# Performance work log

Hardware: AMD Instinct MI355X
Metric: run time of the kernel (lower is better)

## Reference

```python
import jax, jax.numpy as jnp
import numpy as np

B, D, H, O, E = 4096, 1024, 4096, 1024, 8
TOP_K = 2


def setup_inputs() -> dict:
    key = jax.random.key(0)
    ks = jax.random.split(key, 7)
    s = 0.02
    return {
        "expert_input": jax.random.normal(ks[0], (B, D), dtype=jnp.float32),
        "Wg": jax.random.normal(ks[1], (D, E), dtype=jnp.float32) * s,
        "bg": jnp.zeros((E,), dtype=jnp.float32),
        "W1": jax.random.normal(ks[2], (E, D, H), dtype=jnp.float32) * s,
        "b1": jnp.zeros((E, H), dtype=jnp.float32),
        "W2": jax.random.normal(ks[3], (E, H, O), dtype=jnp.float32) * s,
        "b2": jnp.zeros((E, O), dtype=jnp.float32),
    }


def reference(expert_input, Wg, bg, W1, b1, W2, b2):
    x = expert_input                                  # [B, D]
    gate_logits = x @ Wg + bg                         # [B, E]
    topk_logits, topk_idx = jax.lax.top_k(gate_logits, TOP_K)
    topk_w = jax.nn.softmax(topk_logits, axis=1)      # softmax over the k selected logits
    rows = jnp.arange(x.shape[0])[:, None]
    dense_w = jnp.zeros_like(gate_logits).at[rows, topk_idx].set(topk_w)  # [B, E]
    # Dense (all-experts) evaluation; zero gate weight == unrouted, so math
    # matches the masked per-expert loop in the torch module exactly.
    h = jax.nn.relu(jnp.einsum('bd,edh->ebh', x, W1) + b1[:, None, :])    # [E, B, H]
    expert_out = jnp.einsum('ebh,eho->ebo', h, W2) + b2[:, None, :]       # [E, B, O]
    routed = jnp.einsum('be,ebo->bo', dense_w, expert_out)                # [B, O]
    return routed
```

## Files before the change

kernel.cpp:

```cpp
#include <hip/hip_runtime.h>
#include <cstdint>

#define DEVI __device__ __forceinline__

typedef __bf16 bf16x8_t __attribute__((ext_vector_type(8)));
typedef float f32x4_t __attribute__((ext_vector_type(4)));

typedef const __attribute__((address_space(1))) unsigned int* gas_t;
typedef __attribute__((address_space(3))) unsigned int* las_t;

DEVI void glds16(const void* g, void* l) {
  __builtin_amdgcn_global_load_lds((gas_t)g, (las_t)l, 16, 0, 0);
}

DEVI uint16_t f2b(float f) {
  uint32_t u = __builtin_bit_cast(uint32_t, f);
  u += 0x7fffu + ((u >> 16) & 1u);
  return (uint16_t)(u >> 16);
}

DEVI f32x4_t ldsr(uint32_t addr) {
  f32x4_t r;
  asm volatile("ds_read_b128 %0, %1" : "=v"(r) : "v"(addr));
  return r;
}
DEVI f32x4_t ldsr_o(uint32_t addr, int imm) {
  f32x4_t r;
  switch (imm) {
    case 1024: asm volatile("ds_read_b128 %0, %1 offset:1024" : "=v"(r) : "v"(addr)); break;
    case 2048: asm volatile("ds_read_b128 %0, %1 offset:2048" : "=v"(r) : "v"(addr)); break;
    default:   asm volatile("ds_read_b128 %0, %1 offset:3072" : "=v"(r) : "v"(addr)); break;
  }
  return r;
}

static constexpr int MAXT = 72;

__global__ __launch_bounds__(256) void moe_gate(const float* __restrict__ x,
    const float* __restrict__ Wg, const float* __restrict__ bg,
    int* __restrict__ gidx, float* __restrict__ gw) {
  const int lane = threadIdx.x & 63;
  const int b = blockIdx.x * 4 + (threadIdx.x >> 6);
  float acc[8];
#pragma unroll
  for (int e = 0; e < 8; ++e) acc[e] = 0.f;
  const float* xr = x + (size_t)b * 1024;
#pragma unroll
  for (int it = 0; it < 4; ++it) {
    const int d0 = it * 256 + lane * 4;
    float4 xv = *(const float4*)(xr + d0);
    float xs[4] = {xv.x, xv.y, xv.z, xv.w};
#pragma unroll
    for (int q = 0; q < 4; ++q) {
      const float4* wrow = (const float4*)(Wg + (size_t)(d0 + q) * 8);
      float4 wa = wrow[0], wb = wrow[1];
      acc[0] += xs[q] * wa.x; acc[1] += xs[q] * wa.y;
      acc[2] += xs[q] * wa.z; acc[3] += xs[q] * wa.w;
      acc[4] += xs[q] * wb.x; acc[5] += xs[q] * wb.y;
      acc[6] += xs[q] * wb.z; acc[7] += xs[q] * wb.w;
    }
  }
#pragma unroll
  for (int off = 32; off; off >>= 1)
#pragma unroll
    for (int e = 0; e < 8; ++e) acc[e] += __shfl_xor(acc[e], off, 64);
  if (lane == 0) {
    float l[8];
#pragma unroll
    for (int e = 0; e < 8; ++e) l[e] = acc[e] + bg[e];
    int i0 = 0;
#pragma unroll
    for (int e = 1; e < 8; ++e) if (l[e] > l[i0]) i0 = e;
    int i1 = (i0 == 0) ? 1 : 0;
#pragma unroll
    for (int e = 0; e < 8; ++e) if (e != i0 && l[e] > l[i1]) i1 = e;
    float ex = expf(l[i1] - l[i0]);
    float s = 1.f + ex;
    gidx[2 * b] = i0; gidx[2 * b + 1] = i1;
    gw[2 * b] = 1.f / s; gw[2 * b + 1] = ex / s;
  }
}

__global__ __launch_bounds__(256) void moe_scan(const int* __restrict__ gidx,
                                                int* __restrict__ meta) {
  __shared__ int cnt[8];
  if (threadIdx.x < 8) cnt[threadIdx.x] = 0;
  __syncthreads();
  int loc[8] = {0, 0, 0, 0, 0, 0, 0, 0};
  for (int i = threadIdx.x; i < 8192; i += 256) {
    int e = gidx[i];
#pragma unroll
    for (int q = 0; q < 8; ++q) loc[q] += (e == q) ? 1 : 0;
  }
#pragma unroll
  for (int q = 0; q < 8; ++q) atomicAdd(&cnt[q], loc[q]);
  __syncthreads();
  if (threadIdx.x == 0) {
    int off = 0, t = 0;
    for (int e = 0; e < 8; ++e) {
      int c = cnt[e];
      meta[e] = c;
      meta[8 + e] = off;
      meta[17 + e] = 0;
      int nt = (c + 127) >> 7;
      for (int mt = 0; mt < nt; ++mt) {
        meta[32 + t] = e;
        meta[104 + t] = off + mt * 128;
        meta[176 + t] = off + c;
        ++t;
      }
      off += c;
    }
    meta[16] = off;
    meta[25] = t;
  }
}

__global__ __launch_bounds__(256) void moe_scatter(const int* __restrict__ gidx,
    const float* __restrict__ gw, int* __restrict__ meta,
    int* __restrict__ row_index, float* __restrict__ row_w) {
  int i = blockIdx.x * 256 + threadIdx.x;
  int e = gidx[i];
  int pos = meta[8 + e] + atomicAdd(&meta[17 + e], 1);
  row_index[pos] = i >> 1;
  row_w[pos] = gw[i];
}

__global__ __launch_bounds__(256) void moe_cvtx(const float* __restrict__ x,
                                                uint16_t* __restrict__ xb) {
  size_t i = ((size_t)blockIdx.x * 256 + threadIdx.x) * 4;
  float4 v = *(const float4*)(x + i);
  uint64_t pk = (uint64_t)f2b(v.x) | ((uint64_t)f2b(v.y) << 16) |
                ((uint64_t)f2b(v.z) << 32) | ((uint64_t)f2b(v.w) << 48);
  *(uint64_t*)(xb + i) = pk;
}

__global__ __launch_bounds__(256) void moe_transpose(const float* __restrict__ in,
                                                     uint16_t* __restrict__ outp,
                                                     int K, int N) {
  __shared__ uint16_t t[64][72];
  const int e = blockIdx.z;
  const int k0 = blockIdx.y * 64, n0 = blockIdx.x * 64;
  const int r = threadIdx.x >> 2;
  const int c0 = (threadIdx.x & 3) * 16;
  const float* src = in + ((size_t)e * K + k0 + r) * N + n0 + c0;
#pragma unroll
  for (int q = 0; q < 4; ++q) {
    float4 v = *(const float4*)(src + q * 4);
    uint64_t pk = (uint64_t)f2b(v.x) | ((uint64_t)f2b(v.y) << 16) |
                  ((uint64_t)f2b(v.z) << 32) | ((uint64_t)f2b(v.w) << 48);
    *(uint64_t*)&t[r][c0 + q * 4] = pk;
  }
  __syncthreads();
  alignas(16) uint16_t buf[16];
#pragma unroll
  for (int j = 0; j < 16; ++j) buf[j] = t[c0 + j][r];
  uint16_t* dst = outp + ((size_t)e * N + n0 + r) * K + k0 + c0;
  *(uint4*)dst = *(const uint4*)&buf[0];
  *(uint4*)(dst + 8) = *(const uint4*)&buf[8];
}

template <int KD, int ND, int MODE>
__global__ __launch_bounds__(256, 4) void moe_gemm(
    const uint16_t* __restrict__ Am, const uint16_t* __restrict__ Bt,
    const float* __restrict__ bias, const int* __restrict__ meta,
    const int* __restrict__ row_index, const float* __restrict__ row_w,
    uint16_t* __restrict__ hout, float* __restrict__ out) {
  constexpr int NB = ND / 128;
  extern __shared__ uint16_t lds[];
  const int nwg = gridDim.x;
  const int orig = blockIdx.x;
  const int q8 = nwg >> 3, r8 = nwg & 7, xcd = orig & 7, loc = orig >> 3;
  int wg = (xcd < r8 ? xcd * (q8 + 1) : r8 * (q8 + 1) + (xcd - r8) * q8) + loc;
  const int nb = wg % NB;
  const int ty = wg / NB;
  if (ty >= meta[25]) return;
  const int e = meta[32 + ty];
  const int pos0 = meta[104 + ty];
  const int vend = meta[176 + ty];

  const int tid = threadIdx.x;
  const int lane = tid & 63;
  const int w = tid >> 6;
  const int wr = w >> 1, wc = w & 1;

  size_t aoff[2], boff[2];
#pragma unroll
  for (int j = 0; j < 2; ++j) {
    int c = j * 256 + tid;
    int row = c >> 2;
    int skc = (c & 3) ^ ((row >> 1) & 3);
    int pos = pos0 + row;
    if (pos > 8191) pos = 8191;
    int ar = (MODE == 1) ? row_index[pos] : pos;
    aoff[j] = ((size_t)ar * KD + (size_t)skc * 8) * 2;
    boff[j] = (((size_t)e * ND + (size_t)nb * 128 + row) * KD + (size_t)skc * 8) * 2;
  }
  const char* Ag = (const char*)Am;
  const char* Bg = (const char*)Bt;

  auto stage = [&](int s, int kt) {
    uint16_t* Adst = lds + s * 4096;
    uint16_t* Bdst = lds + 16384 + s * 4096;
#pragma unroll
    for (int j = 0; j < 2; ++j) {
      glds16(Ag + aoff[j] + (size_t)kt * 64, Adst + (j * 256 + w * 64) * 8);
      glds16(Bg + boff[j] + (size_t)kt * 64, Bdst + (j * 256 + w * 64) * 8);
    }
  };

  f32x4_t acc[4][4];
  f32x4_t z;
  z[0] = 0.f; z[1] = 0.f; z[2] = 0.f; z[3] = 0.f;
#pragma unroll
  for (int m = 0; m < 4; ++m)
#pragma unroll
    for (int n = 0; n < 4; ++n) acc[m][n] = z;

  const int skcf = ((lane >> 4) ^ ((lane & 15) >> 1)) & 3;
  const uint32_t lbase = (uint32_t)(size_t)&lds[0];
  const uint32_t aFrag = lbase + (uint32_t)(wr * 64 * 32 + (lane & 15) * 32 + skcf * 8) * 2;
  const uint32_t bFrag = lbase + 32768 + (uint32_t)(wc * 64 * 32 + (lane & 15) * 32 + skcf * 8) * 2;

  stage(0, 0); stage(1, 1); stage(2, 2);
  asm volatile("s_waitcnt vmcnt(8)" ::: "memory");
  __builtin_amdgcn_s_barrier();

  const int NIT = KD / 32;
  for (int t = 0; t < NIT; ++t) {
    int tc = t + 3; if (tc > NIT - 1) tc = NIT - 1;
    stage((t + 3) & 3, tc);

    const uint32_t sA = aFrag + (uint32_t)((t & 3) * 8192);
    const uint32_t sB = bFrag + (uint32_t)((t & 3) * 8192);
    f32x4_t a0 = ldsr(sA), a1 = ldsr_o(sA, 1024), a2 = ldsr_o(sA, 2048), a3 = ldsr_o(sA, 3072);
    f32x4_t b0 = ldsr(sB), b1 = ldsr_o(sB, 1024), b2 = ldsr_o(sB, 2048), b3 = ldsr_o(sB, 3072);
    asm volatile("s_waitcnt lgkmcnt(0)" ::: "memory");
    __builtin_amdgcn_sched_barrier(0);

    bf16x8_t af[4] = {__builtin_bit_cast(bf16x8_t, a0), __builtin_bit_cast(bf16x8_t, a1),
                      __builtin_bit_cast(bf16x8_t, a2), __builtin_bit_cast(bf16x8_t, a3)};
    bf16x8_t bfr[4] = {__builtin_bit_cast(bf16x8_t, b0), __builtin_bit_cast(bf16x8_t, b1),
                       __builtin_bit_cast(bf16x8_t, b2), __builtin_bit_cast(bf16x8_t, b3)};
#pragma unroll
    for (int m = 0; m < 4; ++m)
#pragma unroll
      for (int n = 0; n < 4; ++n)
        acc[m][n] = __builtin_amdgcn_mfma_f32_16x16x32_bf16(af[m], bfr[n], acc[m][n], 0, 0, 0);

    asm volatile("s_waitcnt vmcnt(8)" ::: "memory");
    __builtin_amdgcn_s_barrier();
  }
  asm volatile("s_waitcnt vmcnt(0)" ::: "memory");

  const int cb = nb * 128 + wc * 64;
  if constexpr (MODE == 1) {
#pragma unroll
    for (int m = 0; m < 4; ++m) {
      int pr = pos0 + wr * 64 + m * 16 + ((lane >> 4) << 2);
#pragma unroll
      for (int i = 0; i < 4; ++i) {
        int pos = pr + i;
        if (pos < vend) {
#pragma unroll
          for (int n = 0; n < 4; ++n) {
            int col = cb + n * 16 + (lane & 15);
            float v = acc[m][n][i] + bias[e * ND + col];
            v = fmaxf(v, 0.f);
            hout[(size_t)pos * ND + col] = f2b(v);
          }
        }
      }
    }
  } else {
#pragma unroll
    for (int m = 0; m < 4; ++m) {
      int pr = pos0 + wr * 64 + m * 16 + ((lane >> 4) << 2);
#pragma unroll
      for (int i = 0; i < 4; ++i) {
        int pos = pr + i;
        if (pos < vend) {
          int bi = row_index[pos];
          float wgt = row_w[pos];
          float* orow = out + (size_t)bi * ND;
#pragma unroll
          for (int n = 0; n < 4; ++n) {
            int col = cb + n * 16 + (lane & 15);
            float v = (acc[m][n][i] + bias[e * ND + col]) * wgt;
            atomicAdd(orow + col, v);
          }
        }
      }
    }
  }
}

extern "C" void kernel_launch(void* const* d_in, const int* in_sizes, int n_in,
                              void* d_out, int out_size, void* d_ws, size_t ws_size,
                              hipStream_t stream) {
  const float* x  = (const float*)d_in[0];
  const float* Wg = (const float*)d_in[1];
  const float* bg = (const float*)d_in[2];
  const float* W1 = (const float*)d_in[3];
  const float* b1 = (const float*)d_in[4];
  const float* W2 = (const float*)d_in[5];
  const float* b2 = (const float*)d_in[6];
  float* out = (float*)d_out;

  char* ws = (char*)d_ws;
  uint16_t* w1t = (uint16_t*)ws; ws += (size_t)8 * 4096 * 1024 * 2;
  uint16_t* w2t = (uint16_t*)ws; ws += (size_t)8 * 1024 * 4096 * 2;
  uint16_t* xb  = (uint16_t*)ws; ws += (size_t)4096 * 1024 * 2;
  uint16_t* h   = (uint16_t*)ws; ws += (size_t)8192 * 4096 * 2;
  int*   gidx = (int*)ws;   ws += 8192 * 4;
  float* gw   = (float*)ws; ws += 8192 * 4;
  int*   rix  = (int*)ws;   ws += 8192 * 4;
  float* rw   = (float*)ws; ws += 8192 * 4;
  int*   meta = (int*)ws;   ws += 4096;

  hipFuncSetAttribute((const void*)moe_gemm<1024, 4096, 1>,
                      hipFuncAttributeMaxDynamicSharedMemorySize, 65536);
  hipFuncSetAttribute((const void*)moe_gemm<4096, 1024, 2>,
                      hipFuncAttributeMaxDynamicSharedMemorySize, 65536);

  hipMemsetAsync(d_out, 0, (size_t)4096 * 1024 * 4, stream);
  moe_cvtx<<<4096, 256, 0, stream>>>(x, xb);
  moe_transpose<<<dim3(4096 / 64, 1024 / 64, 8), 256, 0, stream>>>(W1, w1t, 1024, 4096);
  moe_transpose<<<dim3(1024 / 64, 4096 / 64, 8), 256, 0, stream>>>(W2, w2t, 4096, 1024);
  moe_gate<<<1024, 256, 0, stream>>>(x, Wg, bg, gidx, gw);
  moe_scan<<<1, 256, 0, stream>>>(gidx, meta);
  moe_scatter<<<32, 256, 0, stream>>>(gidx, gw, meta, rix, rw);
  moe_gemm<1024, 4096, 1><<<dim3(32 * MAXT), 256, 65536, stream>>>(xb, w1t, b1, meta, rix, rw, h, nullptr);
  moe_gemm<4096, 1024, 2><<<dim3(8 * MAXT), 256, 65536, stream>>>(h, w2t, b2, meta, rix, rw, nullptr, out);
}
```

Before: 477.5 us.

## Split-K the second expert GEMM and shrink LDS pipeline to three stages

Adds a split-K template parameter so the down-projection GEMM runs with its K dimension split in two. This doubles the workgroup count and fills the GPU better, and it relies on the existing atomicAdd epilogue, with bias added only by the first slice. The LDS ring buffer drops from four stages to three (48KB instead of 64KB) and launch bounds change from 4 to 3 waves per SIMD. The cost is twice as many atomic adds to the output and shallower prefetch, which may expose more memory latency.

```diff
diff --git a/kernel.cpp b/kernel.cpp
--- a/kernel.cpp
+++ b/kernel.cpp
@@ -160,24 +160,28 @@
   *(uint4*)(dst + 8) = *(const uint4*)&buf[8];
 }
 
-template <int KD, int ND, int MODE>
-__global__ __launch_bounds__(256, 4) void moe_gemm(
+template <int KD, int ND, int MODE, int KSL>
+__global__ __launch_bounds__(256, 3) void moe_gemm(
     const uint16_t* __restrict__ Am, const uint16_t* __restrict__ Bt,
     const float* __restrict__ bias, const int* __restrict__ meta,
     const int* __restrict__ row_index, const float* __restrict__ row_w,
     uint16_t* __restrict__ hout, float* __restrict__ out) {
   constexpr int NB = ND / 128;
+  constexpr int KSLEN = KD / KSL;
+  constexpr int NIT = KSLEN / 32;
   extern __shared__ uint16_t lds[];
   const int nwg = gridDim.x;
   const int orig = blockIdx.x;
   const int q8 = nwg >> 3, r8 = nwg & 7, xcd = orig & 7, loc = orig >> 3;
   int wg = (xcd < r8 ? xcd * (q8 + 1) : r8 * (q8 + 1) + (xcd - r8) * q8) + loc;
-  const int nb = wg % NB;
-  const int ty = wg / NB;
+  const int nb = wg % NB; wg /= NB;
+  const int ks = wg % KSL; wg /= KSL;
+  const int ty = wg;
   if (ty >= meta[25]) return;
   const int e = meta[32 + ty];
   const int pos0 = meta[104 + ty];
   const int vend = meta[176 + ty];
+  const int k0 = ks * KSLEN;
 
   const int tid = threadIdx.x;
   const int lane = tid & 63;
@@ -193,15 +197,15 @@
     int pos = pos0 + row;
     if (pos > 8191) pos = 8191;
     int ar = (MODE == 1) ? row_index[pos] : pos;
-    aoff[j] = ((size_t)ar * KD + (size_t)skc * 8) * 2;
-    boff[j] = (((size_t)e * ND + (size_t)nb * 128 + row) * KD + (size_t)skc * 8) * 2;
+    aoff[j] = ((size_t)ar * KD + (size_t)k0 + (size_t)skc * 8) * 2;
+    boff[j] = (((size_t)e * ND + (size_t)nb * 128 + row) * KD + (size_t)k0 + (size_t)skc * 8) * 2;
   }
   const char* Ag = (const char*)Am;
   const char* Bg = (const char*)Bt;
 
   auto stage = [&](int s, int kt) {
     uint16_t* Adst = lds + s * 4096;
-    uint16_t* Bdst = lds + 16384 + s * 4096;
+    uint16_t* Bdst = lds + 12288 + s * 4096;
 #pragma unroll
     for (int j = 0; j < 2; ++j) {
       glds16(Ag + aoff[j] + (size_t)kt * 64, Adst + (j * 256 + w * 64) * 8);
@@ -220,19 +224,20 @@
   const int skcf = ((lane >> 4) ^ ((lane & 15) >> 1)) & 3;
   const uint32_t lbase = (uint32_t)(size_t)&lds[0];
   const uint32_t aFrag = lbase + (uint32_t)(wr * 64 * 32 + (lane & 15) * 32 + skcf * 8) * 2;
-  const uint32_t bFrag = lbase + 32768 + (uint32_t)(wc * 64 * 32 + (lane & 15) * 32 + skcf * 8) * 2;
-
-  stage(0, 0); stage(1, 1); stage(2, 2);
-  asm volatile("s_waitcnt vmcnt(8)" ::: "memory");
+  const uint32_t bFrag = lbase + 24576 + (uint32_t)(wc * 64 * 32 + (lane & 15) * 32 + skcf * 8) * 2;
+
+  stage(0, 0); stage(1, 1);
+  asm volatile("s_waitcnt vmcnt(4)" ::: "memory");
   __builtin_amdgcn_s_barrier();
 
-  const int NIT = KD / 32;
+  int sRead = 0;
   for (int t = 0; t < NIT; ++t) {
-    int tc = t + 3; if (tc > NIT - 1) tc = NIT - 1;
-    stage((t + 3) & 3, tc);
-
-    const uint32_t sA = aFrag + (uint32_t)((t & 3) * 8192);
-    const uint32_t sB = bFrag + (uint32_t)((t & 3) * 8192);
+    int sW = sRead + 2; if (sW >= 3) sW -= 3;
+    int tc = t + 2; if (tc > NIT - 1) tc = NIT - 1;
+    stage(sW, tc);
+
+    const uint32_t sA = aFrag + (uint32_t)(sRead * 8192);
+    const uint32_t sB = bFrag + (uint32_t)(sRead * 8192);
     f32x4_t a0 = ldsr(sA), a1 = ldsr_o(sA, 1024), a2 = ldsr_o(sA, 2048), a3 = ldsr_o(sA, 3072);
     f32x4_t b0 = ldsr(sB), b1 = ldsr_o(sB, 1024), b2 = ldsr_o(sB, 2048), b3 = ldsr_o(sB, 3072);
     asm volatile("s_waitcnt lgkmcnt(0)" ::: "memory");
@@ -248,8 +253,9 @@
       for (int n = 0; n < 4; ++n)
         acc[m][n] = __builtin_amdgcn_mfma_f32_16x16x32_bf16(af[m], bfr[n], acc[m][n], 0, 0, 0);
 
-    asm volatile("s_waitcnt vmcnt(8)" ::: "memory");
+    asm volatile("s_waitcnt vmcnt(4)" ::: "memory");
     __builtin_amdgcn_s_barrier();
+    sRead = (sRead == 2) ? 0 : sRead + 1;
   }
   asm volatile("s_waitcnt vmcnt(0)" ::: "memory");
 
@@ -286,8 +292,8 @@
 #pragma unroll
           for (int n = 0; n < 4; ++n) {
             int col = cb + n * 16 + (lane & 15);
-            float v = (acc[m][n][i] + bias[e * ND + col]) * wgt;
-            atomicAdd(orow + col, v);
+            float bterm = (ks == 0) ? bias[e * ND + col] : 0.f;
+            atomicAdd(orow + col, (acc[m][n][i] + bterm) * wgt);
           }
         }
       }
@@ -318,10 +324,10 @@
   float* rw   = (float*)ws; ws += 8192 * 4;
   int*   meta = (int*)ws;   ws += 4096;
 
-  hipFuncSetAttribute((const void*)moe_gemm<1024, 4096, 1>,
-                      hipFuncAttributeMaxDynamicSharedMemorySize, 65536);
-  hipFuncSetAttribute((const void*)moe_gemm<4096, 1024, 2>,
-                      hipFuncAttributeMaxDynamicSharedMemorySize, 65536);
+  hipFuncSetAttribute((const void*)moe_gemm<1024, 4096, 1, 1>,
+                      hipFuncAttributeMaxDynamicSharedMemorySize, 49152);
+  hipFuncSetAttribute((const void*)moe_gemm<4096, 1024, 2, 2>,
+                      hipFuncAttributeMaxDynamicSharedMemorySize, 49152);
 
   hipMemsetAsync(d_out, 0, (size_t)4096 * 1024 * 4, stream);
   moe_cvtx<<<4096, 256, 0, stream>>>(x, xb);
@@ -330,6 +336,6 @@
   moe_gate<<<1024, 256, 0, stream>>>(x, Wg, bg, gidx, gw);
   moe_scan<<<1, 256, 0, stream>>>(gidx, meta);
   moe_scatter<<<32, 256, 0, stream>>>(gidx, gw, meta, rix, rw);
-  moe_gemm<1024, 4096, 1><<<dim3(32 * MAXT), 256, 65536, stream>>>(xb, w1t, b1, meta, rix, rw, h, nullptr);
-  moe_gemm<4096, 1024, 2><<<dim3(8 * MAXT), 256, 65536, stream>>>(h, w2t, b2, meta, rix, rw, nullptr, out);
-}
+  moe_gemm<1024, 4096, 1, 1><<<dim3(32 * MAXT), 256, 49152, stream>>>(xb, w1t, b1, meta, rix, rw, h, nullptr);
+  moe_gemm<4096, 1024, 2, 2><<<dim3(8 * 2 * MAXT), 256, 49152, stream>>>(h, w2t, b2, meta, rix, rw, nullptr, out);
+}
```

Measured after the change: 458.1 us. -4.1%, faster.
